# Performance work log

Measured on AMD Instinct MI355X. Metric: run time of the kernel, lower is better.

Reference implementation:

```python
import jax, jax.numpy as jnp
import numpy as np

OBS_X, OBS_Y, RADIUS = 40.0, 15.0, 6.0
B = 524288  # batch of states


def setup_inputs() -> dict:
    key = jax.random.key(0)
    ks = jax.random.split(key, 14)
    def lin_w(k, o, i):
        return jax.random.normal(k, (o, i), jnp.float32) * (1.0 / np.sqrt(i))
    return {
        "x": jax.random.normal(ks[0], (B, 5), jnp.float32),
        "sgn": 1,
        "mean": jax.random.normal(ks[1], (5,), jnp.float32),
        "std": jax.random.uniform(ks[2], (5,), jnp.float32, minval=0.5, maxval=1.5),
        "fc1_w": lin_w(ks[3], 128, 5),
        "fc1_b": jax.random.normal(ks[4], (128,), jnp.float32) * 0.1,
        "fc21_w": lin_w(ks[5], 32, 128),
        "fc21_b": jax.random.normal(ks[6], (32,), jnp.float32) * 0.1,
        "fc22_w": lin_w(ks[7], 32, 128),
        "fc22_b": jax.random.normal(ks[8], (32,), jnp.float32) * 0.1,
        "fc31_w": lin_w(ks[9], 2, 32),
        "fc31_b": jax.random.normal(ks[10], (2,), jnp.float32) * 0.1,
        "fc32_w": lin_w(ks[11], 2, 32),
        "fc32_b": jax.random.normal(ks[12], (2,), jnp.float32) * 0.1,
    }


def reference(x, sgn, mean, std, fc1_w, fc1_b, fc21_w, fc21_b,
              fc22_w, fc22_b, fc31_w, fc31_b, fc32_w, fc32_b):
    # --- tiny MLP (DynamicUnicycle2D config: 5 -> 128 -> {32,32} -> {2,2}) ---
    x0 = x * std + mean                                   # de-normalized state [B,5]
    h1 = jax.nn.relu(x @ fc1_w.T + fc1_b)                 # [B,128]
    x21 = jax.nn.relu(h1 @ fc21_w.T + fc21_b)             # [B,32]
    x22 = jax.nn.relu(h1 @ fc22_w.T + fc22_b)             # [B,32]
    x31 = x21 @ fc31_w.T + fc31_b                         # QP linear cost p, [B,2]
    x32 = 4.0 * jax.nn.sigmoid(x22 @ fc32_w.T + fc32_b)   # CBF class-K gains, [B,2]

    # --- CBF derivation (relative degree 2, circular obstacle) ---
    px, py, theta, v = x0[:, 0], x0[:, 1], x0[:, 2], x0[:, 3]
    s, c = jnp.sin(theta), jnp.cos(theta)
    dx, dy = px - OBS_X, py - OBS_Y
    barrier = dx * dx + dy * dy - RADIUS * RADIUS
    barrier_dot = 2.0 * dx * v * c + 2.0 * dy * v * s
    Lf2b = 2.0 * v * v
    LgLfbu1 = -2.0 * dx * v * s + 2.0 * dy * v * c
    LgLfbu2 = 2.0 * dx * c + 2.0 * dy * s
    G = jnp.stack([-LgLfbu1, -LgLfbu2], axis=1)           # [B,2], single row constraint
    h = Lf2b + (x32[:, 0] + x32[:, 1]) * barrier_dot + x32[:, 0] * x32[:, 1] * barrier  # [B]

    # --- batched QP: min 0.5 u^T u + p^T u  s.t.  G u <= h  (Q = I, one constraint)
    # Exact KKT solution: project unconstrained optimum onto the half-space.
    u0 = -x31                                             # unconstrained optimum
    viol = jnp.sum(G * u0, axis=1) - h                    # [B]
    gg = jnp.sum(G * G, axis=1)                           # [B]
    lam = jnp.maximum(viol, 0.0) / (gg + 1e-12)           # active-set multiplier
    u = u0 - lam[:, None] * G                             # [B,2] safe control
    return u
```

## Files before the change

### kernel.cpp

```cpp
#include <hip/hip_runtime.h>
#include <hip/hip_bf16.h>
#include <math.h>

typedef __attribute__((ext_vector_type(8))) _Float16 half8;
typedef __attribute__((ext_vector_type(2))) _Float16 half2v;
typedef __attribute__((ext_vector_type(4))) float f32x4;

#define OBS_X 40.0f
#define OBS_Y 15.0f
#define RADIUS 6.0f
#define TPW 8
#define GRID 1024

__device__ __forceinline__ half2v pkrtz(float a, float b) {
    return __builtin_bit_cast(half2v, __builtin_amdgcn_cvt_pkrtz(a, b));
}

__device__ __forceinline__ void split8(const float* v, half8& hi, half8& lo) {
#pragma unroll
    for (int j = 0; j < 8; ++j) {
        _Float16 h = (_Float16)v[j];
        hi[j] = h;
        lo[j] = (_Float16)(v[j] - (float)h);
    }
}

__global__ __launch_bounds__(256, 2) void barriernet_fused(
    const float* __restrict__ x,
    const float* __restrict__ mean_, const float* __restrict__ std_,
    const float* __restrict__ w1,  const float* __restrict__ b1,
    const float* __restrict__ w21, const float* __restrict__ b21,
    const float* __restrict__ w22, const float* __restrict__ b22,
    const float* __restrict__ w31, const float* __restrict__ b31,
    const float* __restrict__ w32, const float* __restrict__ b32,
    float* __restrict__ out)
{
    __shared__ unsigned char smem[36864];
    const int tid  = threadIdx.x;
    const int lane = tid & 63;
    const int wv   = tid >> 6;
    const int r16  = lane & 15;
    const int g    = lane >> 4;
    unsigned char* h1hi = smem + wv * 8192;
    unsigned char* h1lo = h1hi + 4096;
    unsigned short* w1h_lds = (unsigned short*)(smem + 32768);
    unsigned short* w1l_lds = w1h_lds + 1024;
    const unsigned swz = ((unsigned)(r16 & 7)) << 4;
    const int slot = blockIdx.x * 4 + wv;

    if (tid < 128) {
        float v[8];
#pragma unroll
        for (int j = 0; j < 5; ++j) v[j] = w1[tid * 5 + j];
        v[5] = b1[tid];
        v[6] = 0.f; v[7] = 0.f;
        half8 hi, lo;
        split8(v, hi, lo);
        *(half8*)(w1h_lds + tid * 8) = hi;
        *(half8*)(w1l_lds + tid * 8) = lo;
    }

    half8 w2h[4][4], w2l[4][4];
#pragma unroll
    for (int t = 0; t < 4; ++t) {
        const int r = 16 * t + r16;
        const float* src = (r < 32) ? (w21 + r * 128) : (w22 + (r - 32) * 128);
#pragma unroll
        for (int kc = 0; kc < 4; ++kc) {
            const float4 f0 = *(const float4*)(src + kc * 32 + g * 8);
            const float4 f1 = *(const float4*)(src + kc * 32 + g * 8 + 4);
            float v[8];
            v[0] = f0.x; v[1] = f0.y; v[2] = f0.z; v[3] = f0.w;
            v[4] = f1.x; v[5] = f1.y; v[6] = f1.z; v[7] = f1.w;
            split8(v, w2h[t][kc], w2l[t][kc]);
        }
    }

    __syncthreads();

    const float m0 = mean_[0], m1 = mean_[1], m2 = mean_[2], m3 = mean_[3];
    const float sd0 = std_[0], sd1 = std_[1], sd2 = std_[2], sd3 = std_[3];
    const float bb31_0 = b31[0], bb31_1 = b31[1], bb32_0 = b32[0], bb32_1 = b32[1];

    half8 bxh = {0,0,0,0,0,0,0,0}, bxl = {0,0,0,0,0,0,0,0};
    if (lane < 16) bxh[5] = (_Float16)1.0f;

    float xa0 = 0.f, xa1 = 0.f, xa2 = 0.f, xa3 = 0.f, xa4 = 0.f;
    if (lane < 16) {
        const float* xr = x + (size_t)(slot * TPW * 16 + r16) * 5;
        xa0 = xr[0]; xa1 = xr[1]; xa2 = xr[2]; xa3 = xr[3]; xa4 = xr[4];
    }

#pragma unroll 1
    for (int it = 0; it < TPW; ++it) {
        const int rowbase = (slot * TPW + it) * 16;

        if (lane < 16) {
            _Float16 h;
            h = (_Float16)xa0; bxh[0] = h; bxl[0] = (_Float16)(xa0 - (float)h);
            h = (_Float16)xa1; bxh[1] = h; bxl[1] = (_Float16)(xa1 - (float)h);
            h = (_Float16)xa2; bxh[2] = h; bxl[2] = (_Float16)(xa2 - (float)h);
            h = (_Float16)xa3; bxh[3] = h; bxl[3] = (_Float16)(xa3 - (float)h);
            h = (_Float16)xa4; bxh[4] = h; bxl[4] = (_Float16)(xa4 - (float)h);
        }
        const float xc0 = xa0, xc1 = xa1, xc2 = xa2, xc3 = xa3;

        if (it + 1 < TPW && lane < 16) {
            const float* xr = x + (size_t)(rowbase + 16 + r16) * 5;
            xa0 = xr[0]; xa1 = xr[1]; xa2 = xr[2]; xa3 = xr[3]; xa4 = xr[4];
        }

#pragma unroll
        for (int t8 = 0; t8 < 8; ++t8) {
            half8 awh = {0,0,0,0,0,0,0,0}, awl = {0,0,0,0,0,0,0,0};
            if (lane < 16) {
                awh = *(const half8*)(w1h_lds + (t8 * 16 + r16) * 8);
                awl = *(const half8*)(w1l_lds + (t8 * 16 + r16) * 8);
            }
            f32x4 acc = {0.f, 0.f, 0.f, 0.f};
            acc = __builtin_amdgcn_mfma_f32_16x16x32_f16(awh, bxl, acc, 0, 0, 0);
            acc = __builtin_amdgcn_mfma_f32_16x16x32_f16(awl, bxh, acc, 0, 0, 0);
            acc = __builtin_amdgcn_mfma_f32_16x16x32_f16(awh, bxh, acc, 0, 0, 0);
            float v0 = fmaxf(acc[0], 0.f), v1 = fmaxf(acc[1], 0.f);
            float v2 = fmaxf(acc[2], 0.f), v3 = fmaxf(acc[3], 0.f);
            half2v hA = pkrtz(v0, v1);
            half2v hB = pkrtz(v2, v3);
            half2v lA = pkrtz(v0 - (float)hA[0], v1 - (float)hA[1]);
            half2v lB = pkrtz(v2 - (float)hB[0], v3 - (float)hB[1]);
            const unsigned off = ((unsigned)(32 * t8 + 8 * g)) ^ swz;
            uint2 ph; ph.x = __builtin_bit_cast(unsigned, hA); ph.y = __builtin_bit_cast(unsigned, hB);
            uint2 pl; pl.x = __builtin_bit_cast(unsigned, lA); pl.y = __builtin_bit_cast(unsigned, lB);
            *(uint2*)(h1hi + r16 * 256 + off) = ph;
            *(uint2*)(h1lo + r16 * 256 + off) = pl;
        }

        asm volatile("" ::: "memory");

        half8 ah[4], al[4];
#pragma unroll
        for (int kc = 0; kc < 4; ++kc) {
            const unsigned off = ((unsigned)(kc * 64 + g * 16)) ^ swz;
            ah[kc] = *(const half8*)(h1hi + r16 * 256 + off);
            al[kc] = *(const half8*)(h1lo + r16 * 256 + off);
        }
        f32x4 acc2[4];
#pragma unroll
        for (int t = 0; t < 4; ++t) {
            const float4 bb2 = (t < 2) ? *(const float4*)(b21 + 16 * t + 4 * g)
                                       : *(const float4*)(b22 + 16 * (t - 2) + 4 * g);
            f32x4 a = {bb2.x, bb2.y, bb2.z, bb2.w};
#pragma unroll
            for (int kc = 0; kc < 4; ++kc) {
                a = __builtin_amdgcn_mfma_f32_16x16x32_f16(w2h[t][kc], al[kc], a, 0, 0, 0);
                a = __builtin_amdgcn_mfma_f32_16x16x32_f16(w2l[t][kc], ah[kc], a, 0, 0, 0);
                a = __builtin_amdgcn_mfma_f32_16x16x32_f16(w2h[t][kc], ah[kc], a, 0, 0, 0);
            }
            acc2[t] = a;
        }

        asm volatile("" ::: "memory");

        const f32x4 wA0 = *(const f32x4*)(w31 + 4 * g);
        const f32x4 wA1 = *(const f32x4*)(w31 + 16 + 4 * g);
        const f32x4 wB0 = *(const f32x4*)(w31 + 32 + 4 * g);
        const f32x4 wB1 = *(const f32x4*)(w31 + 48 + 4 * g);
        const f32x4 wC0 = *(const f32x4*)(w32 + 4 * g);
        const f32x4 wC1 = *(const f32x4*)(w32 + 16 + 4 * g);
        const f32x4 wD0 = *(const f32x4*)(w32 + 32 + 4 * g);
        const f32x4 wD1 = *(const f32x4*)(w32 + 48 + 4 * g);
        float p0 = 0.f, p1 = 0.f, p2 = 0.f, p3 = 0.f;
#pragma unroll
        for (int r = 0; r < 4; ++r) {
            float v0 = fmaxf(acc2[0][r], 0.f), v1 = fmaxf(acc2[1][r], 0.f);
            float v2 = fmaxf(acc2[2][r], 0.f), v3 = fmaxf(acc2[3][r], 0.f);
            p0 += wA0[r] * v0 + wA1[r] * v1;
            p1 += wB0[r] * v0 + wB1[r] * v1;
            p2 += wC0[r] * v2 + wC1[r] * v3;
            p3 += wD0[r] * v2 + wD1[r] * v3;
        }
        p0 += __shfl_xor(p0, 16); p0 += __shfl_xor(p0, 32);
        p1 += __shfl_xor(p1, 16); p1 += __shfl_xor(p1, 32);
        p2 += __shfl_xor(p2, 16); p2 += __shfl_xor(p2, 32);
        p3 += __shfl_xor(p3, 16); p3 += __shfl_xor(p3, 32);

        if (lane < 16) {
            const float a31_0 = p0 + bb31_0, a31_1 = p1 + bb31_1;
            const float a32_0 = p2 + bb32_0, a32_1 = p3 + bb32_1;
            const float s0 = 4.0f / (1.0f + __expf(-a32_0));
            const float s1 = 4.0f / (1.0f + __expf(-a32_1));
            const float px = fmaf(xc0, sd0, m0);
            const float py = fmaf(xc1, sd1, m1);
            const float th = fmaf(xc2, sd2, m2);
            const float v  = fmaf(xc3, sd3, m3);
            float sn, cs; __sincosf(th, &sn, &cs);
            const float dx = px - OBS_X, dy = py - OBS_Y;
            const float barrier     = dx * dx + dy * dy - RADIUS * RADIUS;
            const float barrier_dot = 2.f * dx * v * cs + 2.f * dy * v * sn;
            const float Lf2b = 2.f * v * v;
            const float G0 = 2.f * dx * v * sn - 2.f * dy * v * cs;
            const float G1 = -(2.f * dx * cs + 2.f * dy * sn);
            const float h  = Lf2b + (s0 + s1) * barrier_dot + s0 * s1 * barrier;
            const float u00 = -a31_0, u01 = -a31_1;
            const float viol = G0 * u00 + G1 * u01 - h;
            const float gg   = G0 * G0 + G1 * G1;
            const float lam  = fmaxf(viol, 0.f) / (gg + 1e-12f);
            float2 uo = make_float2(fmaf(-lam, G0, u00), fmaf(-lam, G1, u01));
            ((float2*)out)[rowbase + r16] = uo;
        }
    }
}

extern "C" void kernel_launch(void* const* d_in, const int* in_sizes, int n_in,
                              void* d_out, int out_size, void* d_ws, size_t ws_size,
                              hipStream_t stream) {
    const float* x     = (const float*)d_in[0];
    const float* mean_ = (const float*)d_in[2];
    const float* std_  = (const float*)d_in[3];
    const float* w1    = (const float*)d_in[4];
    const float* b1    = (const float*)d_in[5];
    const float* w21   = (const float*)d_in[6];
    const float* b21   = (const float*)d_in[7];
    const float* w22   = (const float*)d_in[8];
    const float* b22   = (const float*)d_in[9];
    const float* w31   = (const float*)d_in[10];
    const float* b31   = (const float*)d_in[11];
    const float* w32   = (const float*)d_in[12];
    const float* b32   = (const float*)d_in[13];

    barriernet_fused<<<GRID, 256, 0, stream>>>(
        x, mean_, std_, w1, b1, w21, b21, w22, b22, w31, b31, w32, b32,
        (float*)d_out);
}
```

Before: 146.1 us.

## Pack split-fp16 fc1 terms into one MFMA K-dimension and double rows per wave

Puts the hi/lo error-compensation terms of the fc1 layer into different K-groups of a single 16x16x32 MFMA instead of issuing three MFMAs per tile. Each lane group loads either the weight hi, the weight lo or a zero row, and supplies the matching x hi, x lo or zero slice. This removes two MFMAs per tile and the per-lane conditional loads. It also doubles the tiles handled per wave while halving the grid, and pins the fc2 weight registers with an empty asm so they stay resident, at some risk of register pressure.

```diff
diff --git a/kernel.cpp b/kernel.cpp
--- a/kernel.cpp
+++ b/kernel.cpp
@@ -9,8 +9,8 @@
 #define OBS_X 40.0f
 #define OBS_Y 15.0f
 #define RADIUS 6.0f
-#define TPW 8
-#define GRID 1024
+#define TPW 16
+#define GRID 512
 
 __device__ __forceinline__ half2v pkrtz(float a, float b) {
     return __builtin_bit_cast(half2v, __builtin_amdgcn_cvt_pkrtz(a, b));
@@ -23,6 +23,12 @@
         hi[j] = h;
         lo[j] = (_Float16)(v[j] - (float)h);
     }
+}
+
+__device__ __forceinline__ void pin(half8& v) {
+    f32x4 t = __builtin_bit_cast(f32x4, v);
+    asm volatile("" : "+v"(t));
+    v = __builtin_bit_cast(half8, t);
 }
 
 __global__ __launch_bounds__(256, 2) void barriernet_fused(
@@ -35,7 +41,7 @@
     const float* __restrict__ w32, const float* __restrict__ b32,
     float* __restrict__ out)
 {
-    __shared__ unsigned char smem[36864];
+    __shared__ unsigned char smem[36880];
     const int tid  = threadIdx.x;
     const int lane = tid & 63;
     const int wv   = tid >> 6;
@@ -43,8 +49,6 @@
     const int g    = lane >> 4;
     unsigned char* h1hi = smem + wv * 8192;
     unsigned char* h1lo = h1hi + 4096;
-    unsigned short* w1h_lds = (unsigned short*)(smem + 32768);
-    unsigned short* w1l_lds = w1h_lds + 1024;
     const unsigned swz = ((unsigned)(r16 & 7)) << 4;
     const int slot = blockIdx.x * 4 + wv;
 
@@ -56,8 +60,12 @@
         v[6] = 0.f; v[7] = 0.f;
         half8 hi, lo;
         split8(v, hi, lo);
-        *(half8*)(w1h_lds + tid * 8) = hi;
-        *(half8*)(w1l_lds + tid * 8) = lo;
+        *(half8*)(smem + 32768 + tid * 16) = hi;
+        *(half8*)(smem + 34816 + tid * 16) = lo;
+    }
+    if (tid == 128) {
+        half8 z = {0,0,0,0,0,0,0,0};
+        *(half8*)(smem + 36864) = z;
     }
 
     half8 w2h[4][4], w2l[4][4];
@@ -73,6 +81,8 @@
             v[0] = f0.x; v[1] = f0.y; v[2] = f0.z; v[3] = f0.w;
             v[4] = f1.x; v[5] = f1.y; v[6] = f1.z; v[7] = f1.w;
             split8(v, w2h[t][kc], w2l[t][kc]);
+            pin(w2h[t][kc]);
+            pin(w2l[t][kc]);
         }
     }
 
@@ -82,11 +92,11 @@
     const float sd0 = std_[0], sd1 = std_[1], sd2 = std_[2], sd3 = std_[3];
     const float bb31_0 = b31[0], bb31_1 = b31[1], bb32_0 = b32[0], bb32_1 = b32[1];
 
-    half8 bxh = {0,0,0,0,0,0,0,0}, bxl = {0,0,0,0,0,0,0,0};
-    if (lane < 16) bxh[5] = (_Float16)1.0f;
-
-    float xa0 = 0.f, xa1 = 0.f, xa2 = 0.f, xa3 = 0.f, xa4 = 0.f;
-    if (lane < 16) {
+    const unsigned awbase = (g < 2) ? 32768u : ((g == 2) ? 34816u : 36864u);
+    const unsigned awstep = (g == 3) ? 0u : 16u;
+
+    float xa0, xa1, xa2, xa3, xa4;
+    {
         const float* xr = x + (size_t)(slot * TPW * 16 + r16) * 5;
         xa0 = xr[0]; xa1 = xr[1]; xa2 = xr[2]; xa3 = xr[3]; xa4 = xr[4];
     }
@@ -95,32 +105,31 @@
     for (int it = 0; it < TPW; ++it) {
         const int rowbase = (slot * TPW + it) * 16;
 
-        if (lane < 16) {
-            _Float16 h;
-            h = (_Float16)xa0; bxh[0] = h; bxl[0] = (_Float16)(xa0 - (float)h);
-            h = (_Float16)xa1; bxh[1] = h; bxl[1] = (_Float16)(xa1 - (float)h);
-            h = (_Float16)xa2; bxh[2] = h; bxl[2] = (_Float16)(xa2 - (float)h);
-            h = (_Float16)xa3; bxh[3] = h; bxl[3] = (_Float16)(xa3 - (float)h);
-            h = (_Float16)xa4; bxh[4] = h; bxl[4] = (_Float16)(xa4 - (float)h);
+        half8 bx = {0,0,0,0,0,0,0,0};
+        {
+            float xs[5] = {xa0, xa1, xa2, xa3, xa4};
+            const bool useL = (g == 1), useZ = (g == 3);
+#pragma unroll
+            for (int j = 0; j < 5; ++j) {
+                _Float16 h = (_Float16)xs[j];
+                _Float16 l = (_Float16)(xs[j] - (float)h);
+                bx[j] = useZ ? (_Float16)0.f : (useL ? l : h);
+            }
+            bx[5] = (useZ || useL) ? (_Float16)0.f : (_Float16)1.0f;
         }
         const float xc0 = xa0, xc1 = xa1, xc2 = xa2, xc3 = xa3;
 
-        if (it + 1 < TPW && lane < 16) {
+        if (it + 1 < TPW) {
             const float* xr = x + (size_t)(rowbase + 16 + r16) * 5;
             xa0 = xr[0]; xa1 = xr[1]; xa2 = xr[2]; xa3 = xr[3]; xa4 = xr[4];
         }
 
 #pragma unroll
         for (int t8 = 0; t8 < 8; ++t8) {
-            half8 awh = {0,0,0,0,0,0,0,0}, awl = {0,0,0,0,0,0,0,0};
-            if (lane < 16) {
-                awh = *(const half8*)(w1h_lds + (t8 * 16 + r16) * 8);
-                awl = *(const half8*)(w1l_lds + (t8 * 16 + r16) * 8);
-            }
+            const int fr = t8 * 16 + r16;
+            const half8 aw = *(const half8*)(smem + awbase + (unsigned)fr * awstep);
             f32x4 acc = {0.f, 0.f, 0.f, 0.f};
-            acc = __builtin_amdgcn_mfma_f32_16x16x32_f16(awh, bxl, acc, 0, 0, 0);
-            acc = __builtin_amdgcn_mfma_f32_16x16x32_f16(awl, bxh, acc, 0, 0, 0);
-            acc = __builtin_amdgcn_mfma_f32_16x16x32_f16(awh, bxh, acc, 0, 0, 0);
+            acc = __builtin_amdgcn_mfma_f32_16x16x32_f16(aw, bx, acc, 0, 0, 0);
             float v0 = fmaxf(acc[0], 0.f), v1 = fmaxf(acc[1], 0.f);
             float v2 = fmaxf(acc[2], 0.f), v3 = fmaxf(acc[3], 0.f);
             half2v hA = pkrtz(v0, v1);
```

Result: faster. 133.6 us (-8.5%).
